# Performance work log

Measured on AMD Instinct MI355X. Metric: run time of the kernel, lower is better.

Reference implementation:

```python
import jax, jax.numpy as jnp
import numpy as np
from functools import partial

STRIDES = (8, 16, 32)
SCORE_THRESH = 0.3
NMS_THRESH = 0.5
TOPK = 500          # fixed pre-NMS candidate count (jit-friendly substitute for boolean masking)
CLASS_OFFSET = 1e4  # offset boxes per class so cross-class IoU == 0 -> per-class NMS


def _decode(cls, reg, obj, stride):
    # cls [B,C,H,W], reg [B,4,H,W], obj [B,1,H,W]
    B, C, H, W = cls.shape
    yv, xv = jnp.meshgrid(jnp.arange(H, dtype=cls.dtype), jnp.arange(W, dtype=cls.dtype), indexing='ij')
    scores = jax.nn.sigmoid(obj) * jax.nn.sigmoid(cls)          # [B,C,H,W]
    dx, dy, dw, dh = reg[:, 0], reg[:, 1], reg[:, 2], reg[:, 3]
    cx = (xv + jax.nn.sigmoid(dx)) * stride
    cy = (yv + jax.nn.sigmoid(dy)) * stride
    w = jnp.exp(dw) * stride
    h = jnp.exp(dh) * stride
    boxes = jnp.stack([cx - w / 2, cy - h / 2, cx + w / 2, cy + h / 2], axis=-1)  # [B,H,W,4]
    return boxes.reshape(B, H * W, 4), scores.reshape(B, C, H * W).transpose(0, 2, 1)


def _pairwise_iou(boxes):
    # boxes [B,K,4] xyxy -> iou [B,K,K]
    area = (boxes[..., 2] - boxes[..., 0]) * (boxes[..., 3] - boxes[..., 1])
    x1 = jnp.maximum(boxes[:, :, None, 0], boxes[:, None, :, 0])
    y1 = jnp.maximum(boxes[:, :, None, 1], boxes[:, None, :, 1])
    x2 = jnp.minimum(boxes[:, :, None, 2], boxes[:, None, :, 2])
    y2 = jnp.minimum(boxes[:, :, None, 3], boxes[:, None, :, 3])
    inter = jnp.clip(x2 - x1, 0) * jnp.clip(y2 - y1, 0)
    union = area[:, :, None] + area[:, None, :] - inter
    return inter / (union + 1e-7)


def _greedy_nms(iou, valid):
    # iou [B,K,K], valid [B,K] -> keep [B,K]; greedy over score-sorted order (axis 1)
    B, K = valid.shape
    def step(supp, i):
        keep_i = valid[:, i] & ~supp[:, i]                    # [B]
        supp = supp | (keep_i[:, None] & (iou[:, i, :] >= NMS_THRESH))
        return supp, keep_i
    _, keep_t = jax.lax.scan(step, jnp.zeros((B, K), dtype=bool), jnp.arange(K))
    return keep_t.T  # [B,K]


def _predict(levels):
    boxes_l, scores_l = [], []
    for (c, r, o), s in zip(levels, STRIDES):
        b, sc = _decode(c, r, o, s)
        boxes_l.append(b)
        scores_l.append(sc)
    boxes = jnp.concatenate(boxes_l, axis=1)     # [B,N,4]
    scores = jnp.concatenate(scores_l, axis=1)   # [B,N,C]
    max_scores = scores.max(axis=-1)             # [B,N]
    labels = jnp.argmax(scores, axis=-1)         # [B,N]
    masked = jnp.where(max_scores > SCORE_THRESH, max_scores, -1.0)
    top_scores, idx = jax.lax.top_k(masked, TOPK)                         # sorted desc
    top_boxes = jnp.take_along_axis(boxes, idx[..., None], axis=1)        # [B,K,4]
    top_labels = jnp.take_along_axis(labels, idx, axis=1)                 # [B,K]
    valid = top_scores > SCORE_THRESH
    boxes_off = top_boxes + (top_labels.astype(top_boxes.dtype) * CLASS_OFFSET)[..., None]
    keep = _greedy_nms(_pairwise_iou(boxes_off), valid)                   # [B,K]
    out_boxes = jnp.where(keep[..., None], top_boxes, 0.0)
    out_scores = jnp.where(keep, top_scores, 0.0)
    return out_boxes, out_scores, top_labels, keep


def setup_inputs() -> dict:
    key = jax.random.key(0)
    ks = jax.random.split(key, 9)
    B, C = 64, 2
    shapes = {
        'cls_p3': (B, C, 160, 160), 'reg_p3': (B, 4, 160, 160), 'obj_p3': (B, 1, 160, 160),
        'cls_p4': (B, C, 80, 80),   'reg_p4': (B, 4, 80, 80),   'obj_p4': (B, 1, 80, 80),
        'cls_p5': (B, C, 40, 40),   'reg_p5': (B, 4, 40, 40),   'obj_p5': (B, 1, 40, 40),
    }
    return {name: jax.random.normal(k, shp, dtype=jnp.float32)
            for k, (name, shp) in zip(ks, shapes.items())}


def reference(cls_p3, reg_p3, obj_p3, cls_p4, reg_p4, obj_p4, cls_p5, reg_p5, obj_p5):
    levels = [(cls_p3, reg_p3, obj_p3), (cls_p4, reg_p4, obj_p4), (cls_p5, reg_p5, obj_p5)]
    return _predict(levels)
```

## Files before the change

kernel.cpp:

```cpp
#include <hip/hip_runtime.h>
#include <hip/hip_bf16.h>
#include <stdint.h>

#define NB 64
#define NA 33600
#define NK 500
#define HW3 25600
#define HW4 6400
#define HW5 1600
#define OFF4 25600
#define OFF5 32000
#define NA4 8400
#define NSEG 33
#define NBIN 256
#define LCAP 1024
#define MROWS 512

typedef unsigned short u16;
typedef unsigned int u32;
typedef unsigned long long u64;

__device__ __forceinline__ float sigf(float x) { return 1.0f / (1.0f + expf(-x)); }

__device__ __forceinline__ u32 f2key(float f) {
  u32 u = __float_as_uint(f);
  return (u & 0x80000000u) ? ~u : (u | 0x80000000u);
}
__device__ __forceinline__ float key2f(u32 k) {
  u32 u = (k & 0x80000000u) ? (k ^ 0x80000000u) : ~k;
  return __uint_as_float(u);
}
__device__ __forceinline__ int bin_of(float s) {
  int b = (int)(s * 256.0f);
  return b > 255 ? 255 : b;
}
__device__ __forceinline__ u64 uniform64(u64 v) {
  u32 lo = (u32)__builtin_amdgcn_readfirstlane((int)(u32)v);
  u32 hi = (u32)__builtin_amdgcn_readfirstlane((int)(u32)(v >> 32));
  return ((u64)hi << 32) | lo;
}
__device__ __forceinline__ float mscore(float o, float c0, float c1) {
  float so = sigf(o);
  float s = fmaxf(so * sigf(c0), so * sigf(c1));
  return s;
}

__global__ __launch_bounds__(256) void k_hist(
    const float* __restrict__ cls3, const float* __restrict__ obj3,
    const float* __restrict__ cls4, const float* __restrict__ obj4,
    const float* __restrict__ cls5, const float* __restrict__ obj5,
    u16* __restrict__ ghist_part, u32* __restrict__ cnt)
{
  int seg = blockIdx.x, b = blockIdx.y, tid = threadIdx.x;
  int i4 = seg * 256 + tid;
  __shared__ u32 hist[NBIN];
  hist[tid] = 0;
  if (seg == 0 && tid == 0) cnt[b] = 0;
  __syncthreads();

  if (i4 < NA4) {
    const float* cls; const float* obj; int p4, HW;
    if (i4 < 6400)      { cls = cls3; obj = obj3; p4 = i4;        HW = HW3; }
    else if (i4 < 8000) { cls = cls4; obj = obj4; p4 = i4 - 6400; HW = HW4; }
    else                { cls = cls5; obj = obj5; p4 = i4 - 8000; HW = HW5; }
    float4 o  = reinterpret_cast<const float4*>(obj + (size_t)b * HW)[p4];
    float4 c0 = reinterpret_cast<const float4*>(cls + (size_t)(b * 2) * HW)[p4];
    float4 c1 = reinterpret_cast<const float4*>(cls + (size_t)(b * 2 + 1) * HW)[p4];
    float s;
    s = mscore(o.x, c0.x, c1.x); if (s > 0.3f) atomicAdd(&hist[bin_of(s)], 1u);
    s = mscore(o.y, c0.y, c1.y); if (s > 0.3f) atomicAdd(&hist[bin_of(s)], 1u);
    s = mscore(o.z, c0.z, c1.z); if (s > 0.3f) atomicAdd(&hist[bin_of(s)], 1u);
    s = mscore(o.w, c0.w, c1.w); if (s > 0.3f) atomicAdd(&hist[bin_of(s)], 1u);
  }
  __syncthreads();
  if (tid < 128) {
    u32 pk = (hist[2 * tid] & 0xFFFFu) | (hist[2 * tid + 1] << 16);
    reinterpret_cast<u32*>(ghist_part + ((size_t)(b * NSEG + seg) * NBIN))[tid] = pk;
  }
}

__global__ __launch_bounds__(256) void k_collect(
    const float* __restrict__ cls3, const float* __restrict__ obj3,
    const float* __restrict__ cls4, const float* __restrict__ obj4,
    const float* __restrict__ cls5, const float* __restrict__ obj5,
    const u16* __restrict__ ghist_part,
    u64* __restrict__ cand, u32* __restrict__ cnt)
{
  int seg = blockIdx.x, b = blockIdx.y, tid = threadIdx.x;
  __shared__ u32 part[NBIN];
  __shared__ int sh_p;
  __shared__ u64 loc[1024];
  __shared__ u32 lcnt;
  __shared__ u32 gbase;

  u32 sum = 0;
  for (int s2 = 0; s2 < NSEG; ++s2)
    sum += ghist_part[(size_t)(b * NSEG + s2) * NBIN + tid];
  part[tid] = sum;
  if (tid == 0) lcnt = 0;
  __syncthreads();
  for (int off = 1; off < NBIN; off <<= 1) {
    u32 add = (tid + off < NBIN) ? part[tid + off] : 0u;
    __syncthreads();
    part[tid] += add;
    __syncthreads();
  }
  if (tid == 0 && part[0] < NK) sh_p = NBIN;
  u32 S = part[tid];
  u32 Snext = (tid == NBIN - 1) ? 0u : part[tid + 1];
  if (S >= NK && Snext < NK) sh_p = tid;
  __syncthreads();
  int p = sh_p;

  int i4 = seg * 256 + tid;
  if (i4 < NA4) {
    const float* cls; const float* obj; int p4, HW;
    if (i4 < 6400)      { cls = cls3; obj = obj3; p4 = i4;        HW = HW3; }
    else if (i4 < 8000) { cls = cls4; obj = obj4; p4 = i4 - 6400; HW = HW4; }
    else                { cls = cls5; obj = obj5; p4 = i4 - 8000; HW = HW5; }
    float4 o  = reinterpret_cast<const float4*>(obj + (size_t)b * HW)[p4];
    float4 c0 = reinterpret_cast<const float4*>(cls + (size_t)(b * 2) * HW)[p4];
    float4 c1 = reinterpret_cast<const float4*>(cls + (size_t)(b * 2 + 1) * HW)[p4];
    float sv[4];
    sv[0] = mscore(o.x, c0.x, c1.x);
    sv[1] = mscore(o.y, c0.y, c1.y);
    sv[2] = mscore(o.z, c0.z, c1.z);
    sv[3] = mscore(o.w, c0.w, c1.w);
#pragma unroll
    for (int c = 0; c < 4; ++c) {
      float s = sv[c];
      if (s > 0.3f && bin_of(s) >= p) {
        u32 slot = atomicAdd(&lcnt, 1u);
        loc[slot] = ((u64)f2key(s) << 16) | (u32)(0xFFFF - (i4 * 4 + c));
      }
    }
  }
  __syncthreads();
  if (tid == 0) gbase = atomicAdd(&cnt[b], lcnt);
  __syncthreads();
  u32 n = lcnt, gb = gbase;
  for (u32 i = tid; i < n; i += 256) {
    u32 slot = gb + i;
    if (slot < LCAP) cand[(size_t)b * LCAP + slot] = loc[i];
  }
}

__device__ __forceinline__ float anchor_score(
    int b, int a,
    const float* cls3, const float* obj3,
    const float* cls4, const float* obj4,
    const float* cls5, const float* obj5)
{
  const float* cls; const float* obj; int pos, HW;
  if (a < OFF4)      { cls = cls3; obj = obj3; pos = a;        HW = HW3; }
  else if (a < OFF5) { cls = cls4; obj = obj4; pos = a - OFF4; HW = HW4; }
  else               { cls = cls5; obj = obj5; pos = a - OFF5; HW = HW5; }
  return mscore(obj[b * HW + pos], cls[(b * 2) * HW + pos], cls[(b * 2 + 1) * HW + pos]);
}

__global__ __launch_bounds__(512) void k_sortdec(
    const u64* __restrict__ gcand, const u32* __restrict__ cnt,
    const float* __restrict__ cls3, const float* __restrict__ obj3, const float* __restrict__ reg3,
    const float* __restrict__ cls4, const float* __restrict__ obj4, const float* __restrict__ reg4,
    const float* __restrict__ cls5, const float* __restrict__ obj5, const float* __restrict__ reg5,
    float* __restrict__ top_score,
    float4* __restrict__ boxes, float4* __restrict__ boxesoff,
    float* __restrict__ out_labels)
{
  int b = blockIdx.x, tid = threadIdx.x;
  __shared__ u64 cand[LCAP];
  __shared__ int idx_lds[NK];
  __shared__ float score_lds[NK];
  __shared__ u32 hist[256];
  __shared__ u32 part[256];
  __shared__ u32 sh_R;
  __shared__ int sh_digit;
  __shared__ u32 sh_cnt;

  u32 n = cnt[b];
  bool fail = (n < (u32)NK) || (n > LCAP);

  if (!fail) {
    for (int i = tid; i < LCAP; i += 512)
      cand[i] = (i < (int)n) ? gcand[(size_t)b * LCAP + i] : 0ull;
    for (int k = 2; k <= LCAP; k <<= 1) {
      for (int j = k >> 1; j > 0; j >>= 1) {
        __syncthreads();
        int i = ((tid & ~(j - 1)) << 1) | (tid & (j - 1));
        int ixj = i | j;
        u64 a = cand[i], c2 = cand[ixj];
        bool dir = ((i & k) == 0);
        if ((a < c2) == dir) { cand[i] = c2; cand[ixj] = a; }
      }
    }
    __syncthreads();
    if (tid < NK) {
      u64 kk = cand[tid];
      idx_lds[tid] = 0xFFFF - (int)(kk & 0xFFFFull);
      score_lds[tid] = key2f((u32)(kk >> 16));
    }
  } else {
    u64 prefix = 0, prefmask = 0;
    u32 R = NK;
    for (int pass = 0; pass < 6; ++pass) {
      int shift = 40 - 8 * pass;
      if (tid < 256) part[tid] = 0;
      __syncthreads();
      for (int i = tid; i < NA; i += 512) {
        float s = anchor_score(b, i, cls3, obj3, cls4, obj4, cls5, obj5);
        float masked = (s > 0.3f) ? s : -1.0f;
        u64 k48 = ((u64)f2key(masked) << 16) | (u32)(0xFFFF - i);
        if ((k48 & prefmask) == prefix)
          atomicAdd(&part[(u32)(k48 >> shift) & 255u], 1u);
      }
      __syncthreads();
      if (tid < 256) hist[tid] = part[tid];
      __syncthreads();
      for (int off = 1; off < 256; off <<= 1) {
        u32 add = 0;
        if (tid < 256 && tid + off < 256) add = hist[tid + off];
        __syncthreads();
        if (tid < 256) hist[tid] += add;
        __syncthreads();
      }
      if (tid < 256) {
        u32 s = hist[tid];
        u32 snext = (tid == 255) ? 0u : hist[tid + 1];
        if (s >= R && snext < R) { sh_digit = tid; sh_R = R - snext; }
      }
      __syncthreads();
      prefix |= ((u64)sh_digit) << shift;
      R = sh_R;
      prefmask |= 0xFFull << shift;
      __syncthreads();
    }
    if (tid == 0) sh_cnt = 0;
    if (tid < NK) { idx_lds[tid] = 0; score_lds[tid] = -1.0f; }
    __syncthreads();
    for (int i = tid; i < NA; i += 512) {
      float s = anchor_score(b, i, cls3, obj3, cls4, obj4, cls5, obj5);
      float masked = (s > 0.3f) ? s : -1.0f;
      u64 k48 = ((u64)f2key(masked) << 16) | (u32)(0xFFFF - i);
      if (k48 >= prefix) {
        u32 slot = atomicAdd(&sh_cnt, 1u);
        if (slot < 512) cand[slot] = k48;
      }
    }
    __syncthreads();
    int m = (sh_cnt < (u32)NK) ? (int)sh_cnt : NK;
    for (int t = tid; t < m; t += 512) {
      u64 k = cand[t];
      int rank = 0;
      for (int j = 0; j < m; ++j) rank += (cand[j] > k) ? 1 : 0;
      if (rank < NK) {
        idx_lds[rank] = 0xFFFF - (int)(k & 0xFFFFull);
        score_lds[rank] = key2f((u32)(k >> 16));
      }
    }
  }
  __syncthreads();

  if (tid < NK) {
    int a = idx_lds[tid];
    const float *cls, *obj, *reg; int pos, HW, x, y; float stride;
    if (a < OFF4) {
      cls = cls3; obj = obj3; reg = reg3; pos = a; HW = HW3; stride = 8.0f;
      y = pos / 160; x = pos - y * 160;
    } else if (a < OFF5) {
      cls = cls4; obj = obj4; reg = reg4; pos = a - OFF4; HW = HW4; stride = 16.0f;
      y = pos / 80; x = pos - y * 80;
    } else {
      cls = cls5; obj = obj5; reg = reg5; pos = a - OFF5; HW = HW5; stride = 32.0f;
      y = pos / 40; x = pos - y * 40;
    }
    float dx = reg[(b * 4 + 0) * HW + pos];
    float dy = reg[(b * 4 + 1) * HW + pos];
    float dw = reg[(b * 4 + 2) * HW + pos];
    float dh = reg[(b * 4 + 3) * HW + pos];
    float cx = ((float)x + sigf(dx)) * stride;
    float cy = ((float)y + sigf(dy)) * stride;
    float w = expf(dw) * stride;
    float h = expf(dh) * stride;
    float x1 = cx - w * 0.5f, y1 = cy - h * 0.5f;
    float x2 = cx + w * 0.5f, y2 = cy + h * 0.5f;
    float so = sigf(obj[b * HW + pos]);
    float s0 = so * sigf(cls[(b * 2) * HW + pos]);
    float s1 = so * sigf(cls[(b * 2 + 1) * HW + pos]);
    int label = (s1 > s0) ? 1 : 0;
    float off = (float)label * 10000.0f;
    int t = b * NK + tid;
    boxes[t]    = make_float4(x1, y1, x2, y2);
    boxesoff[t] = make_float4(x1 + off, y1 + off, x2 + off, y2 + off);
    out_labels[t] = (float)label;
    top_score[t] = score_lds[tid];
  }
}

__global__ __launch_bounds__(256) void k_iou(
    const float4* __restrict__ boxesoff, u64* __restrict__ mask)
{
  int t = blockIdx.x * 256 + threadIdx.x;
  if (t >= NB * NK * 8) return;
  int w = t & 7;
  int bi = t >> 3;
  int b = bi / NK;
  int i = bi - b * NK;
  float4 A = boxesoff[bi];
  float areaA = (A.z - A.x) * (A.w - A.y);
  const float4* base = boxesoff + b * NK;
  int j0 = w * 64;
  int jmax = (NK - j0 < 64) ? (NK - j0) : 64;
  u64 bits = 0;
  for (int jj = 0; jj < jmax; ++jj) {
    float4 Bx = base[j0 + jj];
    float areaB = (Bx.z - Bx.x) * (Bx.w - Bx.y);
    float ix1 = fmaxf(A.x, Bx.x);
    float iy1 = fmaxf(A.y, Bx.y);
    float ix2 = fminf(A.z, Bx.z);
    float iy2 = fminf(A.w, Bx.w);
    float iw = fmaxf(ix2 - ix1, 0.0f);
    float ih = fmaxf(iy2 - iy1, 0.0f);
    float inter = iw * ih;
    float uni = areaA + areaB - inter;
    float iou = inter / (uni + 1e-7f);
    bits |= ((u64)(iou >= 0.5f)) << jj;
  }
  mask[(size_t)b * (MROWS * 8) + (size_t)i * 8 + w] = bits;
}

__global__ __launch_bounds__(64) void k_nms(
    const u64* __restrict__ mask, const float* __restrict__ top_score,
    const float4* __restrict__ boxes,
    float* __restrict__ out_boxes, float* __restrict__ out_scores,
    float* __restrict__ out_keep)
{
  int b = blockIdx.x;
  int lane = threadIdx.x;
  const u64* mb = mask + (size_t)b * (MROWS * 8);

  u64 rw[8][8];
#pragma unroll
  for (int c = 0; c < 8; ++c) {
    const ulonglong2* rp =
        reinterpret_cast<const ulonglong2*>(mb + (size_t)(c * 64 + lane) * 8);
#pragma unroll
    for (int q = 0; q < 4; ++q) {
      ulonglong2 v = rp[q];
      rw[c][2 * q] = v.x;
      rw[c][2 * q + 1] = v.y;
    }
  }

  u64 validw[8];
#pragma unroll
  for (int c = 0; c < 8; ++c) {
    int r = c * 64 + lane;
    float s = (r < NK) ? top_score[b * NK + r] : -1.0f;
    validw[c] = __ballot(s > 0.3f);
  }

  u64 himask = (lane == 63) ? 0ull : (~0ull << (lane + 1));
  u64 k[8];
#pragma unroll
  for (int w = 0; w < 8; ++w) k[w] = validw[w];

  for (int it = 0; it < 600; ++it) {
    u64 acc[8] = {0, 0, 0, 0, 0, 0, 0, 0};
#pragma unroll
    for (int c = 0; c < 8; ++c) {
      u64 msel = 0ull - ((k[c] >> lane) & 1ull);
      acc[c] |= rw[c][c] & himask & msel;
#pragma unroll
      for (int w = c + 1; w < 8; ++w) acc[w] |= rw[c][w] & msel;
    }
#pragma unroll
    for (int off = 1; off < 64; off <<= 1) {
#pragma unroll
      for (int w = 0; w < 8; ++w)
        acc[w] |= (u64)__shfl_xor((unsigned long long)acc[w], off, 64);
    }
    bool conv = true;
#pragma unroll
    for (int w = 0; w < 8; ++w) {
      u64 nk = validw[w] & ~uniform64(acc[w]);
      conv = conv && (nk == k[w]);
      k[w] = nk;
    }
    if (conv) break;
  }

#pragma unroll
  for (int c = 0; c < 8; ++c) {
    int r = c * 64 + lane;
    if (r < NK) {
      int kp = (int)((k[c] >> lane) & 1ull);
      float4 bx = boxes[b * NK + r];
      float s = top_score[b * NK + r];
      float4 ob;
      ob.x = kp ? bx.x : 0.0f;
      ob.y = kp ? bx.y : 0.0f;
      ob.z = kp ? bx.z : 0.0f;
      ob.w = kp ? bx.w : 0.0f;
      reinterpret_cast<float4*>(out_boxes)[b * NK + r] = ob;
      out_scores[b * NK + r] = kp ? s : 0.0f;
      out_keep[b * NK + r]   = kp ? 1.0f : 0.0f;
    }
  }
}

extern "C" void kernel_launch(void* const* d_in, const int* in_sizes, int n_in,
                              void* d_out, int out_size, void* d_ws, size_t ws_size,
                              hipStream_t stream) {
  const float* cls3 = (const float*)d_in[0];
  const float* reg3 = (const float*)d_in[1];
  const float* obj3 = (const float*)d_in[2];
  const float* cls4 = (const float*)d_in[3];
  const float* reg4 = (const float*)d_in[4];
  const float* obj4 = (const float*)d_in[5];
  const float* cls5 = (const float*)d_in[6];
  const float* reg5 = (const float*)d_in[7];
  const float* obj5 = (const float*)d_in[8];

  char* ws = (char*)d_ws;
  u16*    ghist     = (u16*)   (ws + 0);
  u32*    cnt       = (u32*)   (ws + 1081344);
  u64*    cand      = (u64*)   (ws + 1081600);
  float*  top_score = (float*) (ws + 1605888);
  float4* boxes     = (float4*)(ws + 1733888);
  float4* boxesoff  = (float4*)(ws + 2245888);
  u64*    mask      = (u64*)   (ws + 2757888);

  float* out        = (float*)d_out;
  float* out_boxes  = out;
  float* out_scores = out + 128000;
  float* out_labels = out + 160000;
  float* out_keep   = out + 192000;

  dim3 gfull(NSEG, NB);
  k_hist<<<gfull, 256, 0, stream>>>(cls3, obj3, cls4, obj4, cls5, obj5,
                                    ghist, cnt);
  k_collect<<<gfull, 256, 0, stream>>>(cls3, obj3, cls4, obj4, cls5, obj5,
                                       ghist, cand, cnt);
  k_sortdec<<<NB, 512, 0, stream>>>(cand, cnt,
      cls3, obj3, reg3, cls4, obj4, reg4, cls5, obj5, reg5,
      top_score, boxes, boxesoff, out_labels);
  k_iou<<<(NB * NK * 8 + 255) / 256, 256, 0, stream>>>(boxesoff, mask);
  k_nms<<<NB, 64, 0, stream>>>(mask, top_score, boxes, out_boxes, out_scores, out_keep);
}
```

Before: 88.79 us.

## Drop histogram pass; collect all above-threshold candidates and radix-select in sortdec

```diff
diff --git a/kernel.cpp b/kernel.cpp
--- a/kernel.cpp
+++ b/kernel.cpp
@@ -12,8 +12,8 @@
 #define OFF5 32000
 #define NA4 8400
 #define NSEG 33
-#define NBIN 256
-#define LCAP 1024
+#define SEGCAP 1024
+#define CAPL 12288
 #define MROWS 512
 
 typedef unsigned short u16;
@@ -29,10 +29,6 @@
 __device__ __forceinline__ float key2f(u32 k) {
   u32 u = (k & 0x80000000u) ? (k ^ 0x80000000u) : ~k;
   return __uint_as_float(u);
-}
-__device__ __forceinline__ int bin_of(float s) {
-  int b = (int)(s * 256.0f);
-  return b > 255 ? 255 : b;
 }
 __device__ __forceinline__ u64 uniform64(u64 v) {
   u32 lo = (u32)__builtin_amdgcn_readfirstlane((int)(u32)v);
@@ -41,76 +37,20 @@
 }
 __device__ __forceinline__ float mscore(float o, float c0, float c1) {
   float so = sigf(o);
-  float s = fmaxf(so * sigf(c0), so * sigf(c1));
-  return s;
-}
-
-__global__ __launch_bounds__(256) void k_hist(
-    const float* __restrict__ cls3, const float* __restrict__ obj3,
-    const float* __restrict__ cls4, const float* __restrict__ obj4,
-    const float* __restrict__ cls5, const float* __restrict__ obj5,
-    u16* __restrict__ ghist_part, u32* __restrict__ cnt)
-{
-  int seg = blockIdx.x, b = blockIdx.y, tid = threadIdx.x;
-  int i4 = seg * 256 + tid;
-  __shared__ u32 hist[NBIN];
-  hist[tid] = 0;
-  if (seg == 0 && tid == 0) cnt[b] = 0;
-  __syncthreads();
-
-  if (i4 < NA4) {
-    const float* cls; const float* obj; int p4, HW;
-    if (i4 < 6400)      { cls = cls3; obj = obj3; p4 = i4;        HW = HW3; }
-    else if (i4 < 8000) { cls = cls4; obj = obj4; p4 = i4 - 6400; HW = HW4; }
-    else                { cls = cls5; obj = obj5; p4 = i4 - 8000; HW = HW5; }
-    float4 o  = reinterpret_cast<const float4*>(obj + (size_t)b * HW)[p4];
-    float4 c0 = reinterpret_cast<const float4*>(cls + (size_t)(b * 2) * HW)[p4];
-    float4 c1 = reinterpret_cast<const float4*>(cls + (size_t)(b * 2 + 1) * HW)[p4];
-    float s;
-    s = mscore(o.x, c0.x, c1.x); if (s > 0.3f) atomicAdd(&hist[bin_of(s)], 1u);
-    s = mscore(o.y, c0.y, c1.y); if (s > 0.3f) atomicAdd(&hist[bin_of(s)], 1u);
-    s = mscore(o.z, c0.z, c1.z); if (s > 0.3f) atomicAdd(&hist[bin_of(s)], 1u);
-    s = mscore(o.w, c0.w, c1.w); if (s > 0.3f) atomicAdd(&hist[bin_of(s)], 1u);
-  }
-  __syncthreads();
-  if (tid < 128) {
-    u32 pk = (hist[2 * tid] & 0xFFFFu) | (hist[2 * tid + 1] << 16);
-    reinterpret_cast<u32*>(ghist_part + ((size_t)(b * NSEG + seg) * NBIN))[tid] = pk;
-  }
+  return fmaxf(so * sigf(c0), so * sigf(c1));
 }
 
 __global__ __launch_bounds__(256) void k_collect(
     const float* __restrict__ cls3, const float* __restrict__ obj3,
     const float* __restrict__ cls4, const float* __restrict__ obj4,
     const float* __restrict__ cls5, const float* __restrict__ obj5,
-    const u16* __restrict__ ghist_part,
-    u64* __restrict__ cand, u32* __restrict__ cnt)
+    u64* __restrict__ cand, u32* __restrict__ blockcnt)
 {
   int seg = blockIdx.x, b = blockIdx.y, tid = threadIdx.x;
-  __shared__ u32 part[NBIN];
-  __shared__ int sh_p;
-  __shared__ u64 loc[1024];
+  __shared__ u64 loc[SEGCAP];
   __shared__ u32 lcnt;
-  __shared__ u32 gbase;
-
-  u32 sum = 0;
-  for (int s2 = 0; s2 < NSEG; ++s2)
-    sum += ghist_part[(size_t)(b * NSEG + s2) * NBIN + tid];
-  part[tid] = sum;
   if (tid == 0) lcnt = 0;
   __syncthreads();
-  for (int off = 1; off < NBIN; off <<= 1) {
-    u32 add = (tid + off < NBIN) ? part[tid + off] : 0u;
-    __syncthreads();
-    part[tid] += add;
-    __syncthreads();
-  }
-  if (tid == 0 && part[0] < NK) sh_p = NBIN;
-  u32 S = part[tid];
-  u32 Snext = (tid == NBIN - 1) ? 0u : part[tid + 1];
-  if (S >= NK && Snext < NK) sh_p = tid;
-  __syncthreads();
-  int p = sh_p;
 
   int i4 = seg * 256 + tid;
   if (i4 < NA4) {
@@ -129,20 +69,17 @@
 #pragma unroll
     for (int c = 0; c < 4; ++c) {
       float s = sv[c];
-      if (s > 0.3f && bin_of(s) >= p) {
+      if (s > 0.3f) {
         u32 slot = atomicAdd(&lcnt, 1u);
         loc[slot] = ((u64)f2key(s) << 16) | (u32)(0xFFFF - (i4 * 4 + c));
       }
     }
   }
   __syncthreads();
-  if (tid == 0) gbase = atomicAdd(&cnt[b], lcnt);
-  __syncthreads();
-  u32 n = lcnt, gb = gbase;
-  for (u32 i = tid; i < n; i += 256) {
-    u32 slot = gb + i;
-    if (slot < LCAP) cand[(size_t)b * LCAP + slot] = loc[i];
-  }
+  u32 n = lcnt;
+  u64* dst = cand + (size_t)(b * NSEG + seg) * SEGCAP;
+  for (u32 i = tid; i < n; i += 256) dst[i] = loc[i];
+  if (tid == 0) blockcnt[b * NSEG + seg] = n;
 }
 
 __device__ __forceinline__ float anchor_score(
@@ -159,7 +96,7 @@
 }
 
 __global__ __launch_bounds__(512) void k_sortdec(
-    const u64* __restrict__ gcand, const u32* __restrict__ cnt,
+    const u64* __restrict__ gcand, const u32* __restrict__ blockcnt,
     const float* __restrict__ cls3, const float* __restrict__ obj3, const float* __restrict__ reg3,
     const float* __restrict__ cls4, const float* __restrict__ obj4, const float* __restrict__ reg4,
     const float* __restrict__ cls5, const float* __restrict__ obj5, const float* __restrict__ reg5,
@@ -168,36 +105,88 @@
     float* __restrict__ out_labels)
 {
   int b = blockIdx.x, tid = threadIdx.x;
-  __shared__ u64 cand[LCAP];
+  __shared__ u64 cl[CAPL];
+  __shared__ u64 coll[512];
   __shared__ int idx_lds[NK];
   __shared__ float score_lds[NK];
   __shared__ u32 hist[256];
   __shared__ u32 part[256];
+  __shared__ u32 segoff[NSEG + 1];
   __shared__ u32 sh_R;
   __shared__ int sh_digit;
   __shared__ u32 sh_cnt;
 
-  u32 n = cnt[b];
-  bool fail = (n < (u32)NK) || (n > LCAP);
+  if (tid == 0) {
+    u32 acc = 0;
+    for (int s2 = 0; s2 < NSEG; ++s2) {
+      segoff[s2] = acc;
+      acc += blockcnt[b * NSEG + s2];
+    }
+    segoff[NSEG] = acc;
+  }
+  __syncthreads();
+  u32 n = segoff[NSEG];
+  bool fail = (n < (u32)NK) || (n > (u32)CAPL);
 
   if (!fail) {
-    for (int i = tid; i < LCAP; i += 512)
-      cand[i] = (i < (int)n) ? gcand[(size_t)b * LCAP + i] : 0ull;
-    for (int k = 2; k <= LCAP; k <<= 1) {
-      for (int j = k >> 1; j > 0; j >>= 1) {
+    for (int s2 = 0; s2 < NSEG; ++s2) {
+      u32 base = segoff[s2], c = segoff[s2 + 1] - base;
+      const u64* src = gcand + (size_t)(b * NSEG + s2) * SEGCAP;
+      for (u32 i = tid; i < c; i += 512) cl[base + i] = src[i];
+    }
+    __syncthreads();
+
+    u64 prefix = 0, prefmask = 0;
+    u32 R = NK;
+    for (int pass = 0; pass < 6; ++pass) {
+      int shift = 40 - 8 * pass;
+      if (tid < 256) part[tid] = 0;
+      __syncthreads();
+      for (u32 i = tid; i < n; i += 512) {
+        u64 k48 = cl[i];
+        if ((k48 & prefmask) == prefix)
+          atomicAdd(&part[(u32)(k48 >> shift) & 255u], 1u);
+      }
+      __syncthreads();
+      if (tid < 256) hist[tid] = part[tid];
+      __syncthreads();
+      for (int off = 1; off < 256; off <<= 1) {
+        u32 add = 0;
+        if (tid < 256 && tid + off < 256) add = hist[tid + off];
         __syncthreads();
-        int i = ((tid & ~(j - 1)) << 1) | (tid & (j - 1));
-        int ixj = i | j;
-        u64 a = cand[i], c2 = cand[ixj];
-        bool dir = ((i & k) == 0);
-        if ((a < c2) == dir) { cand[i] = c2; cand[ixj] = a; }
-      }
-    }
+        if (tid < 256) hist[tid] += add;
+        __syncthreads();
+      }
+      if (tid < 256) {
+        u32 s = hist[tid];
+        u32 snext = (tid == 255) ? 0u : hist[tid + 1];
+        if (s >= R && snext < R) { sh_digit = tid; sh_R = R - snext; }
+      }
+      __syncthreads();
+      prefix |= ((u64)sh_digit) << shift;
+      R = sh_R;
+      prefmask |= 0xFFull << shift;
+      __syncthreads();
+    }
+    if (tid == 0) sh_cnt = 0;
     __syncthreads();
-    if (tid < NK) {
-      u64 kk = cand[tid];
-      idx_lds[tid] = 0xFFFF - (int)(kk & 0xFFFFull);
-      score_lds[tid] = key2f((u32)(kk >> 16));
+    for (u32 i = tid; i < n; i += 512) {
+      u64 k48 = cl[i];
+      if (k48 >= prefix) {
+        u32 slot = atomicAdd(&sh_cnt, 1u);
+        if (slot < 512) coll[slot] = k48;
+      }
+    }
+    __syncthreads();
+    int m = (sh_cnt < (u32)NK) ? (int)sh_cnt : NK;
+    for (int t = tid; t < m; t += 512) {
+      u64 k = coll[t];
+      int rank = 0;
+      for (int j = 0; j < m; ++j) rank += (coll[j] > k) ? 1 : 0;
+      if (rank < NK) {
+        idx_lds[rank] = 0xFFFF - (int)(k & 0xFFFFull);
+        score_lds[rank] = key2f((u32)(k >> 16));
+      }
     }
   } else {
     u64 prefix = 0, prefmask = 0;
@@ -243,15 +232,15 @@
       u64 k48 = ((u64)f2key(masked) << 16) | (u32)(0xFFFF - i);
       if (k48 >= prefix) {
         u32 slot = atomicAdd(&sh_cnt, 1u);
-        if (slot < 512) cand[slot] = k48;
+        if (slot < 512) coll[slot] = k48;
       }
     }
     __syncthreads();
     int m = (sh_cnt < (u32)NK) ? (int)sh_cnt : NK;
     for (int t = tid; t < m; t += 512) {
-      u64 k = cand[t];
+      u64 k = coll[t];
       int rank = 0;
-      for (int j = 0; j < m; ++j) rank += (cand[j] > k) ? 1 : 0;
+      for (int j = 0; j < m; ++j) rank += (coll[j] > k) ? 1 : 0;
       if (rank < NK) {
         idx_lds[rank] = 0xFFFF - (int)(k & 0xFFFFull);
         score_lds[rank] = key2f((u32)(k >> 16));
@@ -422,13 +411,12 @@
   const float* obj5 = (const float*)d_in[8];
 
   char* ws = (char*)d_ws;
-  u16*    ghist     = (u16*)   (ws + 0);
-  u32*    cnt       = (u32*)   (ws + 1081344);
-  u64*    cand      = (u64*)   (ws + 1081600);
-  float*  top_score = (float*) (ws + 1605888);
-  float4* boxes     = (float4*)(ws + 1733888);
-  float4* boxesoff  = (float4*)(ws + 2245888);
-  u64*    mask      = (u64*)   (ws + 2757888);
+  u64*    cand      = (u64*)   (ws + 0);
+  u32*    blockcnt  = (u32*)   (ws + 17301504);
+  float*  top_score = (float*) (ws + 17310208);
+  float4* boxes     = (float4*)(ws + 17438208);
+  float4* boxesoff  = (float4*)(ws + 17950208);
+  u64*    mask      = (u64*)   (ws + 18462208);
 
   float* out        = (float*)d_out;
   float* out_boxes  = out;
@@ -437,11 +425,9 @@
   float* out_keep   = out + 192000;
 
   dim3 gfull(NSEG, NB);
-  k_hist<<<gfull, 256, 0, stream>>>(cls3, obj3, cls4, obj4, cls5, obj5,
-                                    ghist, cnt);
   k_collect<<<gfull, 256, 0, stream>>>(cls3, obj3, cls4, obj4, cls5, obj5,
-                                       ghist, cand, cnt);
-  k_sortdec<<<NB, 512, 0, stream>>>(cand, cnt,
+                                       cand, blockcnt);
+  k_sortdec<<<NB, 512, 0, stream>>>(cand, blockcnt,
       cls3, obj3, reg3, cls4, obj4, reg4, cls5, obj5, reg5,
       top_score, boxes, boxesoff, out_labels);
   k_iou<<<(NB * NK * 8 + 255) / 256, 256, 0, stream>>>(boxesoff, mask);
```

Result: slower. 332.2 us (+274.1%).
